# Optimization experiments

Hardware: AMD Instinct MI355X
Metric: run time of the kernel (lower is better)

## Reference

```python
import jax, jax.numpy as jnp
import numpy as np

MULTIRES = 6          # positional-encoding frequencies (get_embedder)
SKIP_LAYER = 4        # skip_in=(4,) in ImplicitNetwork
BETA = 100.0          # Softplus(beta=100)
INV_SQRT2 = float(1.0 / np.sqrt(2.0))
NUM_NETS = 64         # multi displacement networks (clusters)


def embed(x):
    """NeRF positional embedding: [x, sin(2^k x), cos(2^k x)] for k=0..MULTIRES-1.
    x: [N,3] -> [N, 3 + 3*2*MULTIRES] = [N,39]."""
    outs = [x]
    for i in range(MULTIRES):
        f = float(2.0 ** i)
        outs.append(jnp.sin(f * x))
        outs.append(jnp.cos(f * x))
    return jnp.concatenate(outs, axis=-1)


def softplus100(x):
    # numerically stable softplus with beta=100
    return jnp.logaddexp(0.0, BETA * x) / BETA


def _forward(points,
             iW0, ib0, iW1, ib1, iW2, ib2, iW3, ib3, iW4, ib4,
             iW5, ib5, iW6, ib6, iW7, ib7, iW8, ib8,
             dW0, db0, dW1, db1, dW2, db2, dW3, db3,
             mW0, mb0, mW1, mb1, mW2, mb2):
    N = points.shape[0]
    inp = embed(points)  # [N,39]

    # ---- ImplicitNetwork: 9 linears, softplus(beta=100), skip concat at l=4 ----
    iWs = [iW0, iW1, iW2, iW3, iW4, iW5, iW6, iW7, iW8]
    ibs = [ib0, ib1, ib2, ib3, ib4, ib5, ib6, ib7, ib8]
    x = inp
    for l in range(9):
        if l == SKIP_LAYER:
            x = jnp.concatenate([x, inp], axis=1) * INV_SQRT2  # [N,473+39=512]
        x = x @ iWs[l].T + ibs[l]
        if l < 8:
            x = softplus100(x)
    sdf_feat = x  # [N,257] = sdf (1) + feature vector (256)

    # ---- DisplacementNetwork: 4 linears, ReLU on hidden, Tanh output ----
    xd = inp
    for W, b, last in ((dW0, db0, False), (dW1, db1, False), (dW2, db2, False), (dW3, db3, True)):
        xd = xd @ W.T + b
        xd = jnp.tanh(xd) if last else jax.nn.relu(xd)
    disp = xd  # [N,3]

    # ---- MultiDisplacementNetwork: batched per-cluster MLPs via bmm ----
    xm = inp.reshape(NUM_NETS, -1, inp.shape[1])  # [n, N/n, 39]
    xm = jax.nn.relu(jnp.einsum('nbi,noi->nbo', xm, mW0) + mb0[:, None, :])
    xm = jax.nn.relu(jnp.einsum('nbi,noi->nbo', xm, mW1) + mb1[:, None, :])
    xm = jnp.tanh(jnp.einsum('nbi,noi->nbo', xm, mW2) + mb2[:, None, :])
    mdisp = xm.reshape(N, 3)

    return jnp.concatenate([sdf_feat, disp, mdisp], axis=1)  # [N, 263]


def setup_inputs() -> dict:
    key = jax.random.key(0)
    ks = iter(jax.random.split(key, 80))
    N = 32768
    d = {}
    d['points'] = jax.random.uniform(next(ks), (N, 3), jnp.float32, -1.0, 1.0)

    def mk(out, inn):
        W = jax.random.normal(next(ks), (out, inn), jnp.float32) * (1.0 / np.sqrt(inn))
        b = jax.random.normal(next(ks), (out,), jnp.float32) * 0.01
        return W, b

    impl_shapes = [(512, 39), (512, 512), (512, 512), (473, 512), (512, 512),
                   (512, 512), (512, 512), (512, 512), (257, 512)]
    for l, (o, i) in enumerate(impl_shapes):
        d[f'iW{l}'], d[f'ib{l}'] = mk(o, i)

    disp_shapes = [(512, 39), (512, 512), (512, 512), (3, 512)]
    for l, (o, i) in enumerate(disp_shapes):
        d[f'dW{l}'], d[f'db{l}'] = mk(o, i)

    multi_shapes = [(128, 39), (128, 128), (3, 128)]
    for l, (o, i) in enumerate(multi_shapes):
        W = jax.random.normal(next(ks), (NUM_NETS, o, i), jnp.float32) * (1.0 / np.sqrt(i))
        b = jax.random.normal(next(ks), (NUM_NETS, o), jnp.float32) * 0.01
        d[f'mW{l}'], d[f'mb{l}'] = W, b
    return d


def reference(points,
              iW0, ib0, iW1, ib1, iW2, ib2, iW3, ib3, iW4, ib4,
              iW5, ib5, iW6, ib6, iW7, ib7, iW8, ib8,
              dW0, db0, dW1, db1, dW2, db2, dW3, db3,
              mW0, mb0, mW1, mb1, mW2, mb2):
    return _forward(points,
                    iW0, ib0, iW1, ib1, iW2, ib2, iW3, ib3, iW4, ib4,
                    iW5, ib5, iW6, ib6, iW7, ib7, iW8, ib8,
                    dW0, db0, dW1, db1, dW2, db2, dW3, db3,
                    mW0, mb0, mW1, mb1, mW2, mb2)
```

## Files before the change

kernel.cpp:

```cpp
#include <hip/hip_runtime.h>
#include <hip/hip_bf16.h>
#include <stdint.h>

typedef __attribute__((ext_vector_type(8))) short short8;
typedef __attribute__((ext_vector_type(4))) float floatx4;
typedef __attribute__((ext_vector_type(2))) uint uint2v;

#define INV_SQRT2F 0.70710678118654752440f
#define ROWS 128
#define NT 512

__device__ ushort g_wbuf[4259840];

__device__ __forceinline__ ushort f2bf(float f) {
    union { float f; uint32_t u; } c; c.f = f;
    uint32_t x = c.u;
    return (ushort)((x + 0x7fffu + ((x >> 16) & 1u)) >> 16);
}
__device__ __forceinline__ uint pk2bf(float a, float b) {
    union { __hip_bfloat162 h; uint u; } c;
    c.h = __float22bfloat162_rn(make_float2(a, b));
    return c.u;
}
__device__ __forceinline__ float softplus100(float x) {
    float z = 100.f * x;
    return fmaxf(x, 0.f) + __logf(1.f + __expf(-fabsf(z))) * 0.01f;
}
__device__ __forceinline__ void bar_lgkm() {
    asm volatile("s_waitcnt lgkmcnt(0)\n\ts_barrier" ::: "memory");
}
__device__ __forceinline__ int fidx(int K32, int row, int ch) {
    return (((row >> 4) * K32 + (ch >> 5)) * 64 + ((ch >> 3) & 3) * 16 + (row & 15)) * 8 + (ch & 7);
}

struct Seg { const float* s; int off, nout, kw, k32, ttot, nclust; };
struct CvtAll { Seg seg[16]; };

__global__ void k_cvt(CvtAll c) {
    Seg sg = c.seg[blockIdx.y];
    ushort* d = g_wbuf + sg.off;
    const int pcs8 = sg.ttot * sg.k32 * 64;
    const int tot8 = pcs8 * sg.nclust;
    const bool vec = ((sg.kw & 7) == 0);
    for (int i8 = blockIdx.x * blockDim.x + threadIdx.x; i8 < tot8;
         i8 += gridDim.x * blockDim.x) {
        int cl = i8 / pcs8;
        int r = i8 - cl * pcs8;
        int t = r / (sg.k32 * 64);
        int r2 = r - t * (sg.k32 * 64);
        int kc = r2 >> 6;
        int lane = r2 & 63;
        int n = t * 16 + (lane & 15);
        int kb = kc * 32 + (lane >> 4) * 8;
        const float* src = sg.s + (size_t)cl * sg.nout * sg.kw;
        short8 v = {0, 0, 0, 0, 0, 0, 0, 0};
        if (n < sg.nout) {
            if (vec && kb + 8 <= sg.kw) {
                const float4* s4 = (const float4*)(src + (size_t)n * sg.kw + kb);
                float4 a = s4[0], b = s4[1];
                v[0] = (short)f2bf(a.x); v[1] = (short)f2bf(a.y);
                v[2] = (short)f2bf(a.z); v[3] = (short)f2bf(a.w);
                v[4] = (short)f2bf(b.x); v[5] = (short)f2bf(b.y);
                v[6] = (short)f2bf(b.z); v[7] = (short)f2bf(b.w);
            } else {
#pragma unroll
                for (int j = 0; j < 8; ++j) {
                    int k = kb + j;
                    if (k < sg.kw) v[j] = (short)f2bf(src[(size_t)n * sg.kw + k]);
                }
            }
        }
        *(short8*)(d + (size_t)i8 * 8) = v;
    }
}

template<int K32OUT>
__device__ void embedR(short* act, const float* pts, int row0, short* inp_sv) {
    for (int idx = threadIdx.x; idx < ROWS * 64; idx += NT) {
        int row = idx >> 6, col = idx & 63;
        float v = 0.f;
        if (col < 39) {
            int comp = (col < 3) ? col : (col - 3) % 3;
            float x = pts[(row0 + row) * 3 + comp];
            if (col < 3) v = x;
            else {
                int b = col - 3; int fi = b / 6; int r = b % 6;
                float a = x * (float)(1 << fi);
                v = (r < 3) ? __sinf(a) : __cosf(a);
            }
        }
        act[fidx(K32OUT, row, col)] = (short)f2bf(v);
        if (inp_sv && col < 39) inp_sv[row * 40 + col] = (short)f2bf(v * INV_SQRT2F);
    }
}

template<int ACT, int K32IN, int K32OUT, bool FULL>
__device__ void layer_mm(short* act, const ushort* __restrict__ Wf,
                         const float* __restrict__ bias, int Nout, float scale,
                         bool toLds, float* gOut, int gCol0, int gRow0)
{
    const int tid = threadIdx.x;
    const int wave = tid >> 6, lane = tid & 63;
    const int q = lane >> 4, li = lane & 15;
    const int lane8 = lane * 8;
    const int Ttot = FULL ? 32 : ((Nout + 15) >> 4);

    floatx4 acc[4][8];
#pragma unroll
    for (int i = 0; i < 4; ++i)
#pragma unroll
        for (int m = 0; m < 8; ++m) acc[i][m] = (floatx4){0.f, 0.f, 0.f, 0.f};

    bool tv[4]; const ushort* wb[4];
#pragma unroll
    for (int i = 0; i < 4; ++i) {
        int t = wave * 4 + i;
        tv[i] = FULL ? true : (t < Ttot);
        wb[i] = Wf + (size_t)t * K32IN * 512 + lane8;
    }

    if (FULL || tv[0]) {
        auto loadB = [&](int kc, short8* b) {
#pragma unroll
            for (int i = 0; i < 4; ++i)
                if (FULL || tv[i]) b[i] = *(const short8*)(wb[i] + kc * 512);
        };
        auto step = [&](int kc, short8* b) {
#pragma unroll
            for (int h = 0; h < 4; ++h) {
                short8 afr[2];
#pragma unroll
                for (int m2 = 0; m2 < 2; ++m2)
                    afr[m2] = *(const short8*)
                        &act[((h * 2 + m2) * K32IN + kc) * 512 + lane8];
                __builtin_amdgcn_s_setprio(1);
#pragma unroll
                for (int i = 0; i < 4; ++i) {
                    if (!(FULL || tv[i])) continue;
#pragma unroll
                    for (int m2 = 0; m2 < 2; ++m2)
                        acc[i][h * 2 + m2] = __builtin_amdgcn_mfma_f32_16x16x32_bf16(
                            b[i], afr[m2], acc[i][h * 2 + m2], 0, 0, 0);
                }
                __builtin_amdgcn_s_setprio(0);
            }
        };

        short8 b0[4], b1[4];
        loadB(0, b0);
#pragma unroll
        for (int kc = 0; kc < K32IN; kc += 2) {
            if (kc + 1 < K32IN) loadB(kc + 1, b1);
            step(kc, b0);
            if (kc + 2 < K32IN) loadB(kc + 2, b0);
            if (kc + 1 < K32IN) step(kc + 1, b1);
        }
    }
    bar_lgkm();
#pragma unroll
    for (int i = 0; i < 4; ++i) {
        if (!(FULL || tv[i])) continue;
        const int nb = (wave * 4 + i) * 16 + q * 4;
        if (!FULL && nb >= Nout) continue;
        const bool fullN = FULL || (nb + 4) <= Nout;
        float bs[4];
        if (fullN) {
            float4 b4 = *(const float4*)(bias + nb);
            bs[0] = b4.x; bs[1] = b4.y; bs[2] = b4.z; bs[3] = b4.w;
        } else {
#pragma unroll
            for (int r = 0; r < 4; ++r) bs[r] = (nb + r < Nout) ? bias[nb + r] : 0.f;
        }
        const int wbase = ((nb >> 5)) * 512 + ((nb >> 3) & 3) * 128 + li * 8 + (nb & 7);
#pragma unroll
        for (int m = 0; m < 8; ++m) {
            const int row = m * 16 + li;
            float v[4];
#pragma unroll
            for (int r = 0; r < 4; ++r) {
                float x = acc[i][m][r] + bs[r];
                if (ACT == 1) x = softplus100(x);
                else if (ACT == 2) x = fmaxf(x, 0.f);
                else if (ACT == 3) x = tanhf(x);
                v[r] = x * scale;
            }
            if (toLds) {
                if (fullN) {
                    uint2v pk = {pk2bf(v[0], v[1]), pk2bf(v[2], v[3])};
                    *(uint2v*)&act[m * K32OUT * 512 + wbase] = pk;
                } else {
#pragma unroll
                    for (int r = 0; r < 4; ++r)
                        if (nb + r < Nout)
                            act[fidx(K32OUT, row, nb + r)] = (short)f2bf(v[r]);
                }
            } else {
#pragma unroll
                for (int r = 0; r < 4; ++r)
                    if (nb + r < Nout)
                        gOut[(size_t)(gRow0 + row) * 263 + gCol0 + nb + r] = v[r];
            }
        }
    }
}

struct IP { int iw[9]; const float* ib[9]; };
struct DMP { int dw[4]; const float* db[4]; int mw[3]; const float* mb[3]; };
struct AllP { IP ip; DMP dm; };

struct LayerCtx {
    short* act; short* inp_sv; const float* pts; float* out; int row0;
};

__device__ void run_impl(LayerCtx& c, const IP& p) {
    embedR<2>(c.act, c.pts, c.row0, c.inp_sv);
    bar_lgkm();
    layer_mm<1, 2, 16, true>(c.act, g_wbuf + p.iw[0], p.ib[0], 512, 1.f, true, nullptr, 0, 0);
    bar_lgkm();
    layer_mm<1, 16, 16, true>(c.act, g_wbuf + p.iw[1], p.ib[1], 512, 1.f, true, nullptr, 0, 0);
    bar_lgkm();
    layer_mm<1, 16, 16, true>(c.act, g_wbuf + p.iw[2], p.ib[2], 512, 1.f, true, nullptr, 0, 0);
    bar_lgkm();
    layer_mm<1, 16, 16, false>(c.act, g_wbuf + p.iw[3], p.ib[3], 473, INV_SQRT2F, true, nullptr, 0, 0);
    for (int t2 = threadIdx.x; t2 < ROWS * 64; t2 += NT) {
        int row = t2 >> 6, col = t2 & 63;
        if (col < 39) c.act[fidx(16, row, 473 + col)] = c.inp_sv[row * 40 + col];
    }
    bar_lgkm();
    layer_mm<1, 16, 16, true>(c.act, g_wbuf + p.iw[4], p.ib[4], 512, 1.f, true, nullptr, 0, 0);
    bar_lgkm();
    layer_mm<1, 16, 16, true>(c.act, g_wbuf + p.iw[5], p.ib[5], 512, 1.f, true, nullptr, 0, 0);
    bar_lgkm();
    layer_mm<1, 16, 16, true>(c.act, g_wbuf + p.iw[6], p.ib[6], 512, 1.f, true, nullptr, 0, 0);
    bar_lgkm();
    layer_mm<1, 16, 16, true>(c.act, g_wbuf + p.iw[7], p.ib[7], 512, 1.f, true, nullptr, 0, 0);
    bar_lgkm();
    layer_mm<0, 16, 16, false>(c.act, g_wbuf + p.iw[8], p.ib[8], 257, 1.f, false, c.out, 0, c.row0);
}

__device__ void run_dm(LayerCtx& c, const DMP& p, int rpc) {
    const int cl = c.row0 / rpc;
    const ushort* w0 = g_wbuf + p.mw[0] + cl * 8192;
    const ushort* w1 = g_wbuf + p.mw[1] + cl * 16384;
    const ushort* w2 = g_wbuf + p.mw[2] + cl * 2048;
    embedR<2>(c.act, c.pts, c.row0, nullptr);
    bar_lgkm();
    layer_mm<2, 2, 4, false>(c.act, w0, p.mb[0] + cl * 128, 128, 1.f, true, nullptr, 0, 0);
    bar_lgkm();
    layer_mm<2, 4, 4, false>(c.act, w1, p.mb[1] + cl * 128, 128, 1.f, true, nullptr, 0, 0);
    bar_lgkm();
    layer_mm<3, 4, 4, false>(c.act, w2, p.mb[2] + cl * 3, 3, 1.f, false, c.out, 260, c.row0);
    embedR<2>(c.act, c.pts, c.row0, nullptr);
    bar_lgkm();
    layer_mm<2, 2, 16, true>(c.act, g_wbuf + p.dw[0], p.db[0], 512, 1.f, true, nullptr, 0, 0);
    bar_lgkm();
    layer_mm<2, 16, 16, true>(c.act, g_wbuf + p.dw[1], p.db[1], 512, 1.f, true, nullptr, 0, 0);
    bar_lgkm();
    layer_mm<2, 16, 16, true>(c.act, g_wbuf + p.dw[2], p.db[2], 512, 1.f, true, nullptr, 0, 0);
    bar_lgkm();
    layer_mm<3, 16, 16, false>(c.act, g_wbuf + p.dw[3], p.db[3], 3, 1.f, false, c.out, 257, c.row0);
}

__global__ __launch_bounds__(NT, 2) void k_all(const float* __restrict__ pts,
                                               AllP P, float* __restrict__ out,
                                               int rpc) {
    __shared__ __align__(16) short act[ROWS * 512];
    __shared__ short inp_sv[ROWS * 40];
    const int swz = (blockIdx.x & 7) * 32 + (blockIdx.x >> 3);
    LayerCtx c{act, inp_sv, pts, out, swz * ROWS};
    run_impl(c, P.ip);
    run_dm(c, P.dm, rpc);
}

extern "C" void kernel_launch(void* const* d_in, const int* in_sizes, int n_in,
                              void* d_out, int out_size, void* d_ws, size_t ws_size,
                              hipStream_t stream) {
    const float* pts = (const float*)d_in[0];
    float* out = (float*)d_out;
    const int N = in_sizes[0] / 3;
    const int rpc = N / 64;

    const int iN[9] = {512, 512, 512, 473, 512, 512, 512, 512, 257};
    const int iK[9] = {39, 512, 512, 512, 512, 512, 512, 512, 512};
    const int dN[4] = {512, 512, 512, 3};
    const int dK[4] = {39, 512, 512, 512};
    const int mN[3] = {128, 128, 3};
    const int mK[3] = {39, 128, 128};

    CvtAll cv; AllP P;
    int off = 0, seg = 0;
    auto add_seg = [&](const float* src, int nout, int kw, int nclust) -> int {
        int k32 = ((kw + 31) & ~31) / 32;
        int ttot = (nout + 15) >> 4;
        cv.seg[seg].s = src; cv.seg[seg].off = off;
        cv.seg[seg].nout = nout; cv.seg[seg].kw = kw;
        cv.seg[seg].k32 = k32; cv.seg[seg].ttot = ttot; cv.seg[seg].nclust = nclust;
        int my = off;
        off += ttot * k32 * 512 * nclust;
        ++seg;
        return my;
    };
    for (int l = 0; l < 9; ++l) {
        P.ip.iw[l] = add_seg((const float*)d_in[1 + 2 * l], iN[l], iK[l], 1);
        P.ip.ib[l] = (const float*)d_in[2 + 2 * l];
    }
    for (int l = 0; l < 4; ++l) {
        P.dm.dw[l] = add_seg((const float*)d_in[19 + 2 * l], dN[l], dK[l], 1);
        P.dm.db[l] = (const float*)d_in[20 + 2 * l];
    }
    for (int l = 0; l < 3; ++l) {
        P.dm.mw[l] = add_seg((const float*)d_in[27 + 2 * l], mN[l], mK[l], 64);
        P.dm.mb[l] = (const float*)d_in[28 + 2 * l];
    }

    k_cvt<<<dim3(256, 16), 256, 0, stream>>>(cv);
    k_all<<<N / ROWS, NT, 0, stream>>>(pts, P, out, rpc);
}
```

Before: 451.5 us.

## Halve block threads and give each wave an 8x8 MFMA tile per k-step

The block drops from 512 to 256 threads (4 waves), so each wave now owns 8 output column tiles, interleaved across waves, instead of 4. All 8 row fragments of the activations are loaded once per k-chunk and double-buffered together with the weight fragments. This raises MFMA work per LDS and global load, reusing each fragment more. It needs far more accumulator and fragment registers (64 floatx4 accumulators), so launch bounds drop to one block per SM, which risks lower occupancy, less latency hiding, or register spills.

```diff
diff --git a/kernel.cpp b/kernel.cpp
--- a/kernel.cpp
+++ b/kernel.cpp
@@ -8,7 +8,7 @@
 
 #define INV_SQRT2F 0.70710678118654752440f
 #define ROWS 128
-#define NT 512
+#define NT 256
 
 __device__ ushort g_wbuf[4259840];
 
@@ -105,62 +105,56 @@
     const int lane8 = lane * 8;
     const int Ttot = FULL ? 32 : ((Nout + 15) >> 4);
 
-    floatx4 acc[4][8];
-#pragma unroll
-    for (int i = 0; i < 4; ++i)
+    floatx4 acc[8][8];
+#pragma unroll
+    for (int i = 0; i < 8; ++i)
 #pragma unroll
         for (int m = 0; m < 8; ++m) acc[i][m] = (floatx4){0.f, 0.f, 0.f, 0.f};
 
-    bool tv[4]; const ushort* wb[4];
-#pragma unroll
-    for (int i = 0; i < 4; ++i) {
-        int t = wave * 4 + i;
+    bool tv[8]; const ushort* wb[8];
+#pragma unroll
+    for (int i = 0; i < 8; ++i) {
+        int t = wave + 4 * i;
         tv[i] = FULL ? true : (t < Ttot);
         wb[i] = Wf + (size_t)t * K32IN * 512 + lane8;
     }
 
     if (FULL || tv[0]) {
-        auto loadB = [&](int kc, short8* b) {
-#pragma unroll
-            for (int i = 0; i < 4; ++i)
-                if (FULL || tv[i]) b[i] = *(const short8*)(wb[i] + kc * 512);
+        short8 bA[8], bB[8], fA[8], fB[8];
+        auto loadB = [&](int kc, short8* bb) {
+#pragma unroll
+            for (int i = 0; i < 8; ++i)
+                if (FULL || tv[i]) bb[i] = *(const short8*)(wb[i] + kc * 512);
         };
-        auto step = [&](int kc, short8* b) {
-#pragma unroll
-            for (int h = 0; h < 4; ++h) {
-                short8 afr[2];
-#pragma unroll
-                for (int m2 = 0; m2 < 2; ++m2)
-                    afr[m2] = *(const short8*)
-                        &act[((h * 2 + m2) * K32IN + kc) * 512 + lane8];
-                __builtin_amdgcn_s_setprio(1);
-#pragma unroll
-                for (int i = 0; i < 4; ++i) {
-                    if (!(FULL || tv[i])) continue;
-#pragma unroll
-                    for (int m2 = 0; m2 < 2; ++m2)
-                        acc[i][h * 2 + m2] = __builtin_amdgcn_mfma_f32_16x16x32_bf16(
-                            b[i], afr[m2], acc[i][h * 2 + m2], 0, 0, 0);
-                }
-                __builtin_amdgcn_s_setprio(0);
-            }
+        auto loadF = [&](int kc, short8* ff) {
+#pragma unroll
+            for (int m = 0; m < 8; ++m)
+                ff[m] = *(const short8*)&act[(m * K32IN + kc) * 512 + lane8];
         };
-
-        short8 b0[4], b1[4];
-        loadB(0, b0);
-#pragma unroll
+        auto mm = [&](short8* bb, short8* ff) {
+            __builtin_amdgcn_s_setprio(1);
+#pragma unroll
+            for (int m = 0; m < 8; ++m)
+#pragma unroll
+                for (int i = 0; i < 8; ++i)
+                    if (FULL || tv[i])
+                        acc[i][m] = __builtin_amdgcn_mfma_f32_16x16x32_bf16(
+                            bb[i], ff[m], acc[i][m], 0, 0, 0);
+            __builtin_amdgcn_s_setprio(0);
+        };
+        loadB(0, bA); loadF(0, fA);
         for (int kc = 0; kc < K32IN; kc += 2) {
-            if (kc + 1 < K32IN) loadB(kc + 1, b1);
-            step(kc, b0);
-            if (kc + 2 < K32IN) loadB(kc + 2, b0);
-            if (kc + 1 < K32IN) step(kc + 1, b1);
-        }
-    }
-    bar_lgkm();
-#pragma unroll
-    for (int i = 0; i < 4; ++i) {
+            if (kc + 1 < K32IN) { loadB(kc + 1, bB); loadF(kc + 1, fB); }
+            mm(bA, fA);
+            if (kc + 2 < K32IN) { loadB(kc + 2, bA); loadF(kc + 2, fA); }
+            if (kc + 1 < K32IN) mm(bB, fB);
+        }
+    }
+    bar_lgkm();
+#pragma unroll
+    for (int i = 0; i < 8; ++i) {
         if (!(FULL || tv[i])) continue;
-        const int nb = (wave * 4 + i) * 16 + q * 4;
+        const int nb = (wave + 4 * i) * 16 + q * 4;
         if (!FULL && nb >= Nout) continue;
         const bool fullN = FULL || (nb + 4) <= Nout;
         float bs[4];
@@ -261,7 +255,7 @@
     layer_mm<3, 16, 16, false>(c.act, g_wbuf + p.dw[3], p.db[3], 3, 1.f, false, c.out, 257, c.row0);
 }
 
-__global__ __launch_bounds__(NT, 2) void k_all(const float* __restrict__ pts,
+__global__ __launch_bounds__(NT, 1) void k_all(const float* __restrict__ pts,
                                                AllP P, float* __restrict__ out,
                                                int rpc) {
     __shared__ __align__(16) short act[ROWS * 512];
```

Result: slower. 911.3 us (+101.9%).
